# Kernel tuning notes

Measured on AMD Instinct MI355X. Metric: run time of the kernel, lower is better.

The kernel has to match this reference:

```python
import jax, jax.numpy as jnp
import numpy as np

NH = 12  # num_heads

def setup_inputs() -> dict:
    key = jax.random.key(0)
    ks = jax.random.split(key, 8)
    B, N, C = 8, 1024, 768
    d = C // NH  # head_dim == qk_head_dim (qk_head_dim=None)
    s = 0.02
    return {
        "x": jax.random.normal(ks[0], (B, N, C), jnp.float32),
        "Wq": jax.random.normal(ks[1], (C, NH * d), jnp.float32) * s,
        "Wk": jax.random.normal(ks[2], (C, NH * d), jnp.float32) * s,
        "Wv": jax.random.normal(ks[3], (C, C), jnp.float32) * s,
        "Wproj": jax.random.normal(ks[4], (C, C), jnp.float32) * s,
        "proj_b": jax.random.normal(ks[5], (C,), jnp.float32) * s,
        "attn_bias": jax.random.normal(ks[6], (N, N), jnp.float32) * s,
        "head_bias": jax.random.normal(ks[7], (NH, N, N), jnp.float32) * s,
    }

def reference(x, Wq, Wk, Wv, Wproj, proj_b, attn_bias, head_bias):
    B, N, C = x.shape
    d = C // NH
    scale = d ** -0.5
    # projections: [B,N,C] -> [B,nh,N,d]
    q = jnp.einsum('bnc,ce->bne', x, Wq).reshape(B, N, NH, d).transpose(0, 2, 1, 3)
    k = jnp.einsum('bnc,ce->bne', x, Wk).reshape(B, N, NH, d).transpose(0, 2, 1, 3)
    v = jnp.einsum('bnc,ce->bne', x, Wv).reshape(B, N, NH, d).transpose(0, 2, 1, 3)
    # scaled scores + global bias + per-head bias
    scores = jnp.einsum('bhnd,bhmd->bhnm', q * scale, k)
    scores = scores + attn_bias[None, None] + head_bias[None]
    attn = jax.nn.softmax(scores, axis=-1)  # [B,nh,N,N]
    out = jnp.einsum('bhnm,bhmd->bhnd', attn, v)
    out = out.transpose(0, 2, 1, 3).reshape(B, N, C)
    out = jnp.einsum('bnc,ce->bne', out, Wproj) + proj_b
    return out, attn
```

## Files before the change

### kernel.cpp

```cpp
#include <hip/hip_runtime.h>
#include <hip/hip_bf16.h>
#include <cstddef>

#define B_   8
#define N_   1024
#define C_   768
#define NH_  12
#define HD_  64
#define M_   (B_ * N_)

typedef __attribute__((ext_vector_type(8))) short  short8;
typedef __attribute__((ext_vector_type(4))) float  f32x4;

__device__ __forceinline__ unsigned short f2b(float f) {
    union { float f; unsigned u; } v; v.f = f;
    unsigned u = v.u;
    return (unsigned short)((u + 0x7FFFu + ((u >> 16) & 1u)) >> 16);
}
__device__ __forceinline__ float b2f(unsigned short s) {
    union { unsigned u; float f; } v; v.u = ((unsigned)s) << 16;
    return v.f;
}
__device__ __forceinline__ ushort2 pk2(float a, float b) {
    __hip_bfloat162 t = __float22bfloat162_rn(make_float2(a, b));
    return *(ushort2*)&t;
}
__device__ __forceinline__ void gld16(const unsigned short* g, unsigned short* l) {
    __builtin_amdgcn_global_load_lds(
        (const __attribute__((address_space(1))) void*)g,
        (__attribute__((address_space(3))) void*)l, 16, 0, 0);
}

__global__ __launch_bounds__(256) void cast_x_kernel(const float* __restrict__ x,
                                                     unsigned short* __restrict__ xb) {
    const int n4 = M_ * C_ / 4;
    for (int i = blockIdx.x * blockDim.x + threadIdx.x; i < n4; i += gridDim.x * blockDim.x) {
        float4 v = ((const float4*)x)[i];
        ushort2 lo = pk2(v.x, v.y), hi = pk2(v.z, v.w);
        ushort4 o; o.x = lo.x; o.y = lo.y; o.z = hi.x; o.w = hi.y;
        ((ushort4*)xb)[i] = o;
    }
}

__global__ __launch_bounds__(256) void bias_combine_kernel(
    const float* __restrict__ ab, const float* __restrict__ hbias,
    unsigned short* __restrict__ bc) {
    const int total4 = NH_ * N_ * N_ / 4;
    const int qm4 = N_ * N_ / 4;
    for (int i = blockIdx.x * blockDim.x + threadIdx.x; i < total4; i += gridDim.x * blockDim.x) {
        int rem = i % qm4;
        float4 a = ((const float4*)ab)[rem];
        float4 h = ((const float4*)hbias)[i];
        ushort2 lo = pk2(a.x + h.x, a.y + h.y), hi = pk2(a.z + h.z, a.w + h.w);
        ushort4 o; o.x = lo.x; o.y = lo.y; o.z = hi.x; o.w = hi.y;
        ((ushort4*)bc)[i] = o;
    }
}

__global__ __launch_bounds__(256) void transpose_cast_kernel(
    const float* __restrict__ w0, const float* __restrict__ w1,
    const float* __restrict__ w2, const float* __restrict__ w3,
    unsigned short* __restrict__ t0, unsigned short* __restrict__ t1,
    unsigned short* __restrict__ t2, unsigned short* __restrict__ t3) {
    const int z = blockIdx.z;
    const float* src = (z == 0) ? w0 : (z == 1) ? w1 : (z == 2) ? w2 : w3;
    unsigned short* dst = (z == 0) ? t0 : (z == 1) ? t1 : (z == 2) ? t2 : t3;
    __shared__ float tile[32][33];
    const int r0 = blockIdx.y * 32, c0 = blockIdx.x * 32;
    const int tx = threadIdx.x & 31, ty = threadIdx.x >> 5;
    #pragma unroll
    for (int p = 0; p < 4; ++p)
        tile[ty + 8 * p][tx] = src[(size_t)(r0 + ty + 8 * p) * C_ + c0 + tx];
    __syncthreads();
    #pragma unroll
    for (int p = 0; p < 4; ++p)
        dst[(size_t)(c0 + ty + 8 * p) * C_ + r0 + tx] = f2b(tile[tx][ty + 8 * p]);
}

__global__ __launch_bounds__(256) void qkv_gemm(
    const unsigned short* __restrict__ A,
    const unsigned short* __restrict__ W0, const unsigned short* __restrict__ W1,
    const unsigned short* __restrict__ W2,
    unsigned short* __restrict__ o0, unsigned short* __restrict__ o1,
    unsigned short* __restrict__ o2) {
    __shared__ unsigned short As[128 * 32];
    __shared__ unsigned short Bs[128 * 32];
    const int z = blockIdx.z;
    const unsigned short* Bt = (z == 0) ? W0 : (z == 1) ? W1 : W2;
    const int tid = threadIdx.x;
    const int wid = tid >> 6, lane = tid & 63;
    const int ln = lane & 15, g = lane >> 4;
    const int wm = wid >> 1, wn = wid & 1;
    const int bm = blockIdx.y * 128, bn = blockIdx.x * 128;
    const int lrow = lane >> 2, lch = (lane & 3) * 8;

    f32x4 acc[4][4];
    #pragma unroll
    for (int i = 0; i < 4; ++i)
        #pragma unroll
        for (int j = 0; j < 4; ++j) acc[i][j] = (f32x4)0.f;

    for (int k0 = 0; k0 < C_; k0 += 32) {
        #pragma unroll
        for (int p = 0; p < 2; ++p) {
            const int rowbase = (wid + p * 4) * 16;
            gld16(&A [(size_t)(bm + rowbase + lrow) * C_ + k0 + lch], &As[rowbase * 32]);
            gld16(&Bt[(size_t)(bn + rowbase + lrow) * C_ + k0 + lch], &Bs[rowbase * 32]);
        }
        __syncthreads();
        short8 a[4], b[4];
        #pragma unroll
        for (int mt = 0; mt < 4; ++mt)
            a[mt] = *(const short8*)&As[(wm * 64 + mt * 16 + ln) * 32 + g * 8];
        #pragma unroll
        for (int nt = 0; nt < 4; ++nt)
            b[nt] = *(const short8*)&Bs[(wn * 64 + nt * 16 + ln) * 32 + g * 8];
        #pragma unroll
        for (int mt = 0; mt < 4; ++mt)
            #pragma unroll
            for (int nt = 0; nt < 4; ++nt)
                acc[mt][nt] = __builtin_amdgcn_mfma_f32_16x16x32_bf16(
                    a[mt], b[nt], acc[mt][nt], 0, 0, 0);
        __syncthreads();
    }

    unsigned short* outp = (z == 0) ? o0 : (z == 1) ? o1 : o2;
    #pragma unroll
    for (int mt = 0; mt < 4; ++mt) {
        #pragma unroll
        for (int nt = 0; nt < 4; ++nt) {
            f32x4 c = acc[mt][nt];
            int rowb = bm + wm * 64 + mt * 16 + g * 4;
            int col  = bn + wn * 64 + nt * 16 + ln;
            int hh = col >> 6, dd = col & 63;
            if (z < 2) {
                #pragma unroll
                for (int i = 0; i < 4; ++i) {
                    int row = rowb + i;
                    int bb = row >> 10, n = row & 1023;
                    outp[((size_t)(bb * NH_ + hh) * N_ + n) * HD_ + dd] = f2b(c[i]);
                }
            } else {
                int bb = rowb >> 10, n0 = rowb & 1023;
                ushort2 lo = pk2(c[0], c[1]), hi = pk2(c[2], c[3]);
                ushort4 pk; pk.x = lo.x; pk.y = lo.y; pk.z = hi.x; pk.w = hi.y;
                *(ushort4*)&outp[((size_t)(bb * NH_ + hh) * HD_ + dd) * N_ + n0] = pk;
            }
        }
    }
}

__global__ __launch_bounds__(256) void proj_gemm(
    const unsigned short* __restrict__ A, const unsigned short* __restrict__ Bt,
    const float* __restrict__ bias, float* __restrict__ outp) {
    __shared__ unsigned short As[128 * 32];
    __shared__ unsigned short Bs[128 * 32];
    const int tid = threadIdx.x;
    const int wid = tid >> 6, lane = tid & 63;
    const int ln = lane & 15, g = lane >> 4;
    const int wm = wid >> 1, wn = wid & 1;
    const int bm = blockIdx.y * 128, bn = blockIdx.x * 128;
    const int lrow = lane >> 2, lch = (lane & 3) * 8;

    f32x4 acc[4][4];
    #pragma unroll
    for (int i = 0; i < 4; ++i)
        #pragma unroll
        for (int j = 0; j < 4; ++j) acc[i][j] = (f32x4)0.f;

    for (int k0 = 0; k0 < C_; k0 += 32) {
        #pragma unroll
        for (int p = 0; p < 2; ++p) {
            const int rowbase = (wid + p * 4) * 16;
            gld16(&A [(size_t)(bm + rowbase + lrow) * C_ + k0 + lch], &As[rowbase * 32]);
            gld16(&Bt[(size_t)(bn + rowbase + lrow) * C_ + k0 + lch], &Bs[rowbase * 32]);
        }
        __syncthreads();
        short8 a[4], b[4];
        #pragma unroll
        for (int mt = 0; mt < 4; ++mt)
            a[mt] = *(const short8*)&As[(wm * 64 + mt * 16 + ln) * 32 + g * 8];
        #pragma unroll
        for (int nt = 0; nt < 4; ++nt)
            b[nt] = *(const short8*)&Bs[(wn * 64 + nt * 16 + ln) * 32 + g * 8];
        #pragma unroll
        for (int mt = 0; mt < 4; ++mt)
            #pragma unroll
            for (int nt = 0; nt < 4; ++nt)
                acc[mt][nt] = __builtin_amdgcn_mfma_f32_16x16x32_bf16(
                    a[mt], b[nt], acc[mt][nt], 0, 0, 0);
        __syncthreads();
    }

    #pragma unroll
    for (int mt = 0; mt < 4; ++mt) {
        #pragma unroll
        for (int nt = 0; nt < 4; ++nt) {
            f32x4 c = acc[mt][nt];
            int rowb = bm + wm * 64 + mt * 16 + g * 4;
            int col  = bn + wn * 64 + nt * 16 + ln;
            float bb = bias[col];
            #pragma unroll
            for (int i = 0; i < 4; ++i)
                outp[(size_t)(rowb + i) * C_ + col] = c[i] + bb;
        }
    }
}

__global__ __launch_bounds__(512) void attn_fused(
    const unsigned short* __restrict__ qh, const unsigned short* __restrict__ kh,
    const unsigned short* __restrict__ vt,
    const unsigned short* __restrict__ bias_c,
    float* __restrict__ attn_out, unsigned short* __restrict__ hb) {
    __shared__ unsigned short sc[32 * 1024];
    __shared__ float sinv[32];
    const int id = blockIdx.x;
    const int xcd = id & 7;
    const int b = (id >> 3) & 7;
    const int qbh = ((id >> 6) << 3) + xcd;
    const int qb0 = (qbh / NH_) * 32;
    const int h = qbh % NH_;
    const int bh = b * NH_ + h;
    const int tid = threadIdx.x;
    const int wid = tid >> 6, lane = tid & 63;
    const int ln = lane & 15, g = lane >> 4;

    #define SCP(row, m) ((unsigned short*)((char*)sc + (row) * 2048 + \
                         (((m) * 2) ^ (((row) & 7) << 4))))

    {
        short8 qf[2][2];
        #pragma unroll
        for (int Mt = 0; Mt < 2; ++Mt)
            #pragma unroll
            for (int kc = 0; kc < 2; ++kc)
                qf[Mt][kc] = *(const short8*)&qh[
                    ((size_t)bh * N_ + qb0 + Mt * 16 + ln) * HD_ + kc * 32 + g * 8];
        const int mb = wid * 128;
        const unsigned short* kbase = kh + (size_t)bh * N_ * HD_;
        short8 k0 = *(const short8*)&kbase[(size_t)(mb + ln) * HD_ + g * 8];
        short8 k1 = *(const short8*)&kbase[(size_t)(mb + ln) * HD_ + 32 + g * 8];
        for (int mt = 0; mt < 8; ++mt) {
            const int m0 = mb + mt * 16;
            const int m1 = (mt < 7) ? m0 + 16 : m0;
            short8 n0 = *(const short8*)&kbase[(size_t)(m1 + ln) * HD_ + g * 8];
            short8 n1 = *(const short8*)&kbase[(size_t)(m1 + ln) * HD_ + 32 + g * 8];
            #pragma unroll
            for (int Mt = 0; Mt < 2; ++Mt) {
                f32x4 s = (f32x4)0.f;
                s = __builtin_amdgcn_mfma_f32_16x16x32_bf16(k0, qf[Mt][0], s, 0, 0, 0);
                s = __builtin_amdgcn_mfma_f32_16x16x32_bf16(k1, qf[Mt][1], s, 0, 0, 0);
                const int mrow = m0 + g * 4;
                ushort2 lo = pk2(s[0] * 0.125f, s[1] * 0.125f);
                ushort2 hi = pk2(s[2] * 0.125f, s[3] * 0.125f);
                ushort4 pk; pk.x = lo.x; pk.y = lo.y; pk.z = hi.x; pk.w = hi.y;
                *(ushort4*)SCP(Mt * 16 + ln, mrow) = pk;
            }
            k0 = n0; k1 = n1;
        }
    }
    __syncthreads();

    {
        const int r = tid >> 4, t16 = tid & 15;
        const unsigned short* brow = bias_c + ((size_t)h * N_ + qb0 + r) * N_;
        f32x4 sv[16];
        float mx = -1e30f;
        #pragma unroll
        for (int j = 0; j < 16; ++j) {
            ushort4 er = *(const ushort4*)SCP(r, t16 * 4 + j * 64);
            ushort4 bb = *(const ushort4*)&brow[t16 * 4 + j * 64];
            sv[j][0] = b2f(er.x) + b2f(bb.x);
            sv[j][1] = b2f(er.y) + b2f(bb.y);
            sv[j][2] = b2f(er.z) + b2f(bb.z);
            sv[j][3] = b2f(er.w) + b2f(bb.w);
            mx = fmaxf(fmaxf(fmaxf(mx, sv[j][0]), fmaxf(sv[j][1], sv[j][2])), sv[j][3]);
        }
        #pragma unroll
        for (int off = 8; off; off >>= 1) mx = fmaxf(mx, __shfl_xor(mx, off, 16));
        float sum = 0.f;
        #pragma unroll
        for (int j = 0; j < 16; ++j) {
            float e0 = __expf(sv[j][0] - mx);
            float e1 = __expf(sv[j][1] - mx);
            float e2 = __expf(sv[j][2] - mx);
            float e3 = __expf(sv[j][3] - mx);
            sv[j][0] = e0; sv[j][1] = e1; sv[j][2] = e2; sv[j][3] = e3;
            sum += (e0 + e1) + (e2 + e3);
            ushort2 lo = pk2(e0, e1), hi = pk2(e2, e3);
            ushort4 pk; pk.x = lo.x; pk.y = lo.y; pk.z = hi.x; pk.w = hi.y;
            *(ushort4*)SCP(r, t16 * 4 + j * 64) = pk;
        }
        #pragma unroll
        for (int off = 8; off; off >>= 1) sum += __shfl_xor(sum, off, 16);
        const float inv = 1.f / sum;
        if (t16 == 0) sinv[r] = inv;
        float* arow = attn_out + ((size_t)bh * N_ + qb0 + r) * N_;
        #pragma unroll
        for (int j = 0; j < 16; ++j) {
            f32x4 o;
            o[0] = sv[j][0] * inv; o[1] = sv[j][1] * inv;
            o[2] = sv[j][2] * inv; o[3] = sv[j][3] * inv;
            __builtin_nontemporal_store(o, (f32x4*)&arow[t16 * 4 + j * 64]);
        }
    }
    __syncthreads();

    {
        const int Mt = wid >> 2, nt = wid & 3;
        const unsigned short* vrow = vt + ((size_t)bh * HD_ + nt * 16 + ln) * N_;
        f32x4 acc = (f32x4)0.f;
        short8 pa = *(const short8*)SCP(Mt * 16 + ln, g * 8);
        short8 vb = *(const short8*)&vrow[g * 8];
        for (int kt = 0; kt < 32; ++kt) {
            const int knext = (kt < 31) ? kt + 1 : kt;
            short8 npa = *(const short8*)SCP(Mt * 16 + ln, knext * 32 + g * 8);
            short8 nvb = *(const short8*)&vrow[knext * 32 + g * 8];
            acc = __builtin_amdgcn_mfma_f32_16x16x32_bf16(pa, vb, acc, 0, 0, 0);
            pa = npa; vb = nvb;
        }
        #pragma unroll
        for (int i = 0; i < 4; ++i) {
            int q = qb0 + Mt * 16 + g * 4 + i;
            float o = acc[i] * sinv[Mt * 16 + g * 4 + i];
            hb[(size_t)((b << 10) + q) * C_ + h * HD_ + nt * 16 + ln] = f2b(o);
        }
    }
    #undef SCP
}

extern "C" void kernel_launch(void* const* d_in, const int* in_sizes, int n_in,
                              void* d_out, int out_size, void* d_ws, size_t ws_size,
                              hipStream_t stream) {
    const float* x         = (const float*)d_in[0];
    const float* Wq        = (const float*)d_in[1];
    const float* Wk        = (const float*)d_in[2];
    const float* Wv        = (const float*)d_in[3];
    const float* Wproj     = (const float*)d_in[4];
    const float* proj_b    = (const float*)d_in[5];
    const float* attn_bias = (const float*)d_in[6];
    const float* head_bias = (const float*)d_in[7];

    float* out  = (float*)d_out;
    float* attn = out + (size_t)B_ * N_ * C_;

    unsigned short* ws = (unsigned short*)d_ws;
    const size_t SZ_X = (size_t)M_ * C_;
    const size_t SZ_W = (size_t)C_ * C_;
    unsigned short* xb  = ws;
    unsigned short* wqt = xb + SZ_X;
    unsigned short* wkt = wqt + SZ_W;
    unsigned short* wvt = wkt + SZ_W;
    unsigned short* wpt = wvt + SZ_W;
    unsigned short* qh  = wpt + SZ_W;
    unsigned short* khd = qh + SZ_X;
    unsigned short* vtp = khd + SZ_X;
    unsigned short* bc  = vtp + SZ_X;
    unsigned short* hb  = xb;

    cast_x_kernel<<<2048, 256, 0, stream>>>(x, xb);
    bias_combine_kernel<<<2048, 256, 0, stream>>>(attn_bias, head_bias, bc);
    transpose_cast_kernel<<<dim3(24, 24, 4), 256, 0, stream>>>(
        Wq, Wk, Wv, Wproj, wqt, wkt, wvt, wpt);

    qkv_gemm<<<dim3(C_ / 128, M_ / 128, 3), 256, 0, stream>>>(
        xb, wqt, wkt, wvt, qh, khd, vtp);

    attn_fused<<<dim3(B_ * (N_ / 32) * NH_), 512, 0, stream>>>(
        qh, khd, vtp, bc, attn, hb);

    proj_gemm<<<dim3(C_ / 128, M_ / 128), 256, 0, stream>>>(hb, wpt, proj_b, out);
}
```

Baseline: 299.0 us.

## Interleave attention-probability stores with the PV MFMA loop

Moves the normalized fp32 attention-matrix stores out of the softmax phase and into the unrolled P·V MFMA loop, so the large global writes overlap with matrix-core work. The per-row reciprocal is now read back from shared memory after the barrier. It also adds a min-blocks hint of 4 to launch_bounds. Keeping sv[16] live across the PV loop raises register pressure, and the occupancy hint may force spills.

```diff
diff --git a/kernel.cpp b/kernel.cpp
--- a/kernel.cpp
+++ b/kernel.cpp
@@ -207,7 +207,7 @@
     }
 }
 
-__global__ __launch_bounds__(512) void attn_fused(
+__global__ __launch_bounds__(512, 4) void attn_fused(
     const unsigned short* __restrict__ qh, const unsigned short* __restrict__ kh,
     const unsigned short* __restrict__ vt,
     const unsigned short* __restrict__ bias_c,
@@ -261,14 +261,14 @@
     }
     __syncthreads();
 
+    f32x4 sv[16];
+    const int r2 = tid >> 4, t16 = tid & 15;
     {
-        const int r = tid >> 4, t16 = tid & 15;
-        const unsigned short* brow = bias_c + ((size_t)h * N_ + qb0 + r) * N_;
-        f32x4 sv[16];
+        const unsigned short* brow = bias_c + ((size_t)h * N_ + qb0 + r2) * N_;
         float mx = -1e30f;
         #pragma unroll
         for (int j = 0; j < 16; ++j) {
-            ushort4 er = *(const ushort4*)SCP(r, t16 * 4 + j * 64);
+            ushort4 er = *(const ushort4*)SCP(r2, t16 * 4 + j * 64);
             ushort4 bb = *(const ushort4*)&brow[t16 * 4 + j * 64];
             sv[j][0] = b2f(er.x) + b2f(bb.x);
             sv[j][1] = b2f(er.y) + b2f(bb.y);
@@ -289,35 +289,44 @@
             sum += (e0 + e1) + (e2 + e3);
             ushort2 lo = pk2(e0, e1), hi = pk2(e2, e3);
             ushort4 pk; pk.x = lo.x; pk.y = lo.y; pk.z = hi.x; pk.w = hi.y;
-            *(ushort4*)SCP(r, t16 * 4 + j * 64) = pk;
+            *(ushort4*)SCP(r2, t16 * 4 + j * 64) = pk;
         }
         #pragma unroll
         for (int off = 8; off; off >>= 1) sum += __shfl_xor(sum, off, 16);
-        const float inv = 1.f / sum;
-        if (t16 == 0) sinv[r] = inv;
-        float* arow = attn_out + ((size_t)bh * N_ + qb0 + r) * N_;
-        #pragma unroll
-        for (int j = 0; j < 16; ++j) {
-            f32x4 o;
-            o[0] = sv[j][0] * inv; o[1] = sv[j][1] * inv;
-            o[2] = sv[j][2] * inv; o[3] = sv[j][3] * inv;
-            __builtin_nontemporal_store(o, (f32x4*)&arow[t16 * 4 + j * 64]);
-        }
+        if (t16 == 0) sinv[r2] = 1.f / sum;
     }
     __syncthreads();
 
     {
+        const float invr = sinv[r2];
+        float* arow = attn_out + ((size_t)bh * N_ + qb0 + r2) * N_ + t16 * 4;
         const int Mt = wid >> 2, nt = wid & 3;
         const unsigned short* vrow = vt + ((size_t)bh * HD_ + nt * 16 + ln) * N_;
         f32x4 acc = (f32x4)0.f;
         short8 pa = *(const short8*)SCP(Mt * 16 + ln, g * 8);
         short8 vb = *(const short8*)&vrow[g * 8];
-        for (int kt = 0; kt < 32; ++kt) {
-            const int knext = (kt < 31) ? kt + 1 : kt;
-            short8 npa = *(const short8*)SCP(Mt * 16 + ln, knext * 32 + g * 8);
-            short8 nvb = *(const short8*)&vrow[knext * 32 + g * 8];
-            acc = __builtin_amdgcn_mfma_f32_16x16x32_bf16(pa, vb, acc, 0, 0, 0);
-            pa = npa; vb = nvb;
+        #pragma unroll
+        for (int kt2 = 0; kt2 < 16; ++kt2) {
+            {
+                const int kn = 2 * kt2 + 1;
+                short8 npa = *(const short8*)SCP(Mt * 16 + ln, kn * 32 + g * 8);
+                short8 nvb = *(const short8*)&vrow[kn * 32 + g * 8];
+                acc = __builtin_amdgcn_mfma_f32_16x16x32_bf16(pa, vb, acc, 0, 0, 0);
+                pa = npa; vb = nvb;
+            }
+            {
+                f32x4 o;
+                o[0] = sv[kt2][0] * invr; o[1] = sv[kt2][1] * invr;
+                o[2] = sv[kt2][2] * invr; o[3] = sv[kt2][3] * invr;
+                __builtin_nontemporal_store(o, (f32x4*)&arow[kt2 * 64]);
+            }
+            {
+                const int kn = (kt2 < 15) ? 2 * kt2 + 2 : 2 * kt2 + 1;
+                short8 npa = *(const short8*)SCP(Mt * 16 + ln, kn * 32 + g * 8);
+                short8 nvb = *(const short8*)&vrow[kn * 32 + g * 8];
+                acc = __builtin_amdgcn_mfma_f32_16x16x32_bf16(pa, vb, acc, 0, 0, 0);
+                pa = npa; vb = nvb;
+            }
         }
         #pragma unroll
         for (int i = 0; i < 4; ++i) {
```

After: 293.6 us. No clear change (-1.8%).
